# Kernel tuning notes

Hardware: AMD Instinct MI355X
Metric: run time of the kernel (lower is better)

## Reference

```python
import jax, jax.numpy as jnp
import numpy as np


def setup_inputs() -> dict:
    key = jax.random.key(0)
    k1, k2 = jax.random.split(key)
    x = jax.random.normal(k1, (16384, 1024), dtype=jnp.float32)
    # 10 butterfly stages, each with 512 independent 2x2 mixing matrices
    Ws = jax.random.normal(k2, (10, 512, 2, 2), dtype=jnp.float32)
    return {"x": x, "Ws": Ws}


def reference(x, Ws):
    """PairLinear_MixerBlock forward for input_dim == output_dim == 2^L.
    selector and reducer are Identity; only the butterfly mixing stages remain.
    """
    bs, dim = x.shape
    n_stages = Ws.shape[0]  # log2(dim)
    y = x
    for i in range(n_stages):
        stride = 2 ** i
        # y.view(-1, 2, 2**i).permute(0, 2, 1).contiguous().view(bs, -1)
        y = y.reshape(-1, 2, stride).transpose(0, 2, 1).reshape(bs, -1)
        # PairLinear: view(bs, -1, 2) then per-pair 2x2 matmul with Ws[i]
        y = jnp.einsum('bpk,pkj->bpj', y.reshape(bs, -1, 2), Ws[i]).reshape(bs, -1)
        # y.view(-1, 2**i, 2).permute(0, 2, 1).contiguous()
        y = y.reshape(-1, stride, 2).transpose(0, 2, 1).reshape(bs, dim)
    return y
```

## Files before the change

### kernel.cpp

```cpp
#include <hip/hip_runtime.h>

#define DIM 1024
#define RPW 2
#define WAVES 4
#define ROWS_PER_BLOCK (RPW * WAVES)
#define PACKED_BYTES (6 * 4 * 64 * 8 * 4)

typedef float f32x4 __attribute__((ext_vector_type(4)));


__global__ void pack_weights(const float* __restrict__ Ws, float* __restrict__ pw) {
    int t = blockIdx.x * blockDim.x + threadIdx.x;
    if (t >= 6 * 4 * 64) return;
    int lane = t & 63;
    int q = (t >> 6) & 3;
    int i = (t >> 8) + 2;
    int m = 1 << (i - 2);
    int a = (lane >> (i - 2)) & 1;
    int P0 = (((q * 64 + lane) >> (i - 1)) << i) | ((lane & (m - 1)) << 2);
    const float4* Wm = (const float4*)Ws;
    float4 wa, wb;
    float* pa = (float*)&wa;
    float* pb = (float*)&wb;
    #pragma unroll
    for (int e = 0; e < 4; ++e) {
        float4 M = Wm[i * 512 + P0 + e];
        pa[e] = a ? M.w : M.x;
        pb[e] = a ? M.y : M.z;
    }
    float4* o = (float4*)pw + (size_t)t * 2;
    o[0] = wa;
    o[1] = wb;
}

template <bool PACKED>
__global__ __launch_bounds__(256) void butterfly_kernel(
    const float* __restrict__ x,
    const float* __restrict__ Ws,
    const float* __restrict__ pw,
    float* __restrict__ out,
    int rows)
{
    const int lane = threadIdx.x & 63;
    const int wave = threadIdx.x >> 6;
    const int row0 = (blockIdx.x * WAVES + wave) * RPW;

    const float4* __restrict__ Wm = (const float4*)Ws;

    float d[RPW][16];

    #pragma unroll
    for (int r = 0; r < RPW; ++r) {
        int row = row0 + r;
        if (row < rows) {
            const f32x4* src = (const f32x4*)(x + (size_t)row * DIM);
            #pragma unroll
            for (int q = 0; q < 4; ++q) {
                f32x4 v = __builtin_nontemporal_load(&src[q * 64 + lane]);
                d[r][q*4+0] = v.x; d[r][q*4+1] = v.y;
                d[r][q*4+2] = v.z; d[r][q*4+3] = v.w;
            }
        } else {
            #pragma unroll
            for (int e = 0; e < 16; ++e) d[r][e] = 0.f;
        }
    }

    #pragma unroll
    for (int q = 0; q < 4; ++q) {
        int base = 0*512 + q*128 + lane*2;
        float4 m0 = Wm[base], m1 = Wm[base+1];
        #pragma unroll
        for (int r = 0; r < RPW; ++r) {
            int e = q*4;
            float u = d[r][e+0], v = d[r][e+1];
            d[r][e+0] = u*m0.x + v*m0.z;
            d[r][e+1] = u*m0.y + v*m0.w;
            u = d[r][e+2]; v = d[r][e+3];
            d[r][e+2] = u*m1.x + v*m1.z;
            d[r][e+3] = u*m1.y + v*m1.w;
        }
    }

    #pragma unroll
    for (int q = 0; q < 4; ++q) {
        int base = 1*512 + q*128 + lane*2;
        float4 m0 = Wm[base], m1 = Wm[base+1];
        #pragma unroll
        for (int r = 0; r < RPW; ++r) {
            int e = q*4;
            float u = d[r][e+0], v = d[r][e+2];
            d[r][e+0] = u*m0.x + v*m0.z;
            d[r][e+2] = u*m0.y + v*m0.w;
            u = d[r][e+1]; v = d[r][e+3];
            d[r][e+1] = u*m1.x + v*m1.z;
            d[r][e+3] = u*m1.y + v*m1.w;
        }
    }

    #pragma unroll
    for (int i = 2; i < 8; ++i) {
        const int m = 1 << (i - 2);
        #pragma unroll
        for (int q = 0; q < 4; ++q) {
            float wA0, wA1, wA2, wA3, wB0, wB1, wB2, wB3;
            if (PACKED) {
                const float4* wp = (const float4*)pw
                    + ((size_t)(((i - 2) * 4 + q) * 64 + lane)) * 2;
                float4 wa = wp[0], wb = wp[1];
                wA0 = wa.x; wA1 = wa.y; wA2 = wa.z; wA3 = wa.w;
                wB0 = wb.x; wB1 = wb.y; wB2 = wb.z; wB3 = wb.w;
            } else {
                const int a = (lane >> (i - 2)) & 1;
                int P0 = (((q*64 + lane) >> (i-1)) << i) | ((lane & (m-1)) << 2);
                int base = i*512 + P0;
                float4 M0 = Wm[base+0], M1 = Wm[base+1], M2 = Wm[base+2], M3 = Wm[base+3];
                wA0 = a ? M0.w : M0.x; wB0 = a ? M0.y : M0.z;
                wA1 = a ? M1.w : M1.x; wB1 = a ? M1.y : M1.z;
                wA2 = a ? M2.w : M2.x; wB2 = a ? M2.y : M2.z;
                wA3 = a ? M3.w : M3.x; wB3 = a ? M3.y : M3.z;
            }
            #pragma unroll
            for (int r = 0; r < RPW; ++r) {
                int e = q*4;
                float o0 = __shfl_xor(d[r][e+0], m);
                float o1 = __shfl_xor(d[r][e+1], m);
                float o2 = __shfl_xor(d[r][e+2], m);
                float o3 = __shfl_xor(d[r][e+3], m);
                d[r][e+0] = d[r][e+0]*wA0 + o0*wB0;
                d[r][e+1] = d[r][e+1]*wA1 + o1*wB1;
                d[r][e+2] = d[r][e+2]*wA2 + o2*wB2;
                d[r][e+3] = d[r][e+3]*wA3 + o3*wB3;
            }
        }
    }

    #pragma unroll
    for (int qp = 0; qp < 2; ++qp) {
        int base = 8*512 + qp*256 + lane*4;
        float4 M0 = Wm[base+0], M1 = Wm[base+1], M2 = Wm[base+2], M3 = Wm[base+3];
        #pragma unroll
        for (int r = 0; r < RPW; ++r) {
            int eu = (2*qp)*4, ev = (2*qp+1)*4;
            float u, v;
            u = d[r][eu+0]; v = d[r][ev+0]; d[r][eu+0] = u*M0.x + v*M0.z; d[r][ev+0] = u*M0.y + v*M0.w;
            u = d[r][eu+1]; v = d[r][ev+1]; d[r][eu+1] = u*M1.x + v*M1.z; d[r][ev+1] = u*M1.y + v*M1.w;
            u = d[r][eu+2]; v = d[r][ev+2]; d[r][eu+2] = u*M2.x + v*M2.z; d[r][ev+2] = u*M2.y + v*M2.w;
            u = d[r][eu+3]; v = d[r][ev+3]; d[r][eu+3] = u*M3.x + v*M3.z; d[r][ev+3] = u*M3.y + v*M3.w;
        }
    }

    #pragma unroll
    for (int qp = 0; qp < 2; ++qp) {
        int base = 9*512 + qp*256 + lane*4;
        float4 M0 = Wm[base+0], M1 = Wm[base+1], M2 = Wm[base+2], M3 = Wm[base+3];
        #pragma unroll
        for (int r = 0; r < RPW; ++r) {
            int eu = qp*4, ev = (qp+2)*4;
            float u, v;
            u = d[r][eu+0]; v = d[r][ev+0]; d[r][eu+0] = u*M0.x + v*M0.z; d[r][ev+0] = u*M0.y + v*M0.w;
            u = d[r][eu+1]; v = d[r][ev+1]; d[r][eu+1] = u*M1.x + v*M1.z; d[r][ev+1] = u*M1.y + v*M1.w;
            u = d[r][eu+2]; v = d[r][ev+2]; d[r][eu+2] = u*M2.x + v*M2.z; d[r][ev+2] = u*M2.y + v*M2.w;
            u = d[r][eu+3]; v = d[r][ev+3]; d[r][eu+3] = u*M3.x + v*M3.z; d[r][ev+3] = u*M3.y + v*M3.w;
        }
    }

    #pragma unroll
    for (int r = 0; r < RPW; ++r) {
        int row = row0 + r;
        if (row < rows) {
            f32x4* dst = (f32x4*)(out + (size_t)row * DIM);
            #pragma unroll
            for (int q = 0; q < 4; ++q) {
                f32x4 v;
                v.x = d[r][q*4+0]; v.y = d[r][q*4+1];
                v.z = d[r][q*4+2]; v.w = d[r][q*4+3];
                __builtin_nontemporal_store(v, &dst[q * 64 + lane]);
            }
        }
    }
}

extern "C" void kernel_launch(void* const* d_in, const int* in_sizes, int n_in,
                              void* d_out, int out_size, void* d_ws, size_t ws_size,
                              hipStream_t stream) {
    const float* x  = (const float*)d_in[0];
    const float* Ws = (const float*)d_in[1];
    float* out = (float*)d_out;

    int rows = in_sizes[0] / DIM;
    int grid = (rows + ROWS_PER_BLOCK - 1) / ROWS_PER_BLOCK;

    if (ws_size >= (size_t)PACKED_BYTES) {
        float* pw = (float*)d_ws;
        pack_weights<<<6, 256, 0, stream>>>(Ws, pw);
        butterfly_kernel<true><<<grid, 256, 0, stream>>>(x, Ws, pw, out, rows);
    } else {
        butterfly_kernel<false><<<grid, 256, 0, stream>>>(x, Ws, nullptr, out, rows);
    }
}
```

Before: 47.00 us.

## Process two 4-row tiles per wave with loads issued before compute

Restructures the kernel so each wave owns two tiles of four rows, loading both tiles up front and then computing and storing each in turn. This amortizes per-stage weight loads across more rows and puts more global loads in flight per wave. In exchange it greatly raises register use and shrinks the grid, reducing occupancy. It also drops handling for row counts not divisible by four.

New measurement: 49.95 us. +6.3%, slower.

```diff
diff --git a/kernel.cpp b/kernel.cpp
--- a/kernel.cpp
+++ b/kernel.cpp
@@ -1,9 +1,9 @@
 #include <hip/hip_runtime.h>
 
 #define DIM 1024
-#define RPW 2
+#define RPT 4
 #define WAVES 4
-#define ROWS_PER_BLOCK (RPW * WAVES)
+#define TILES_PER_WAVE 2
 #define PACKED_BYTES (6 * 4 * 64 * 8 * 4)
 
 typedef float f32x4 __attribute__((ext_vector_type(4)));
@@ -33,45 +33,46 @@
     o[1] = wb;
 }
 
+__device__ __forceinline__ void load_tile(const float* __restrict__ x, int tile,
+                                          int lane, float (&d)[RPT][16]) {
+    const f32x4* src = (const f32x4*)(x + (size_t)tile * RPT * DIM);
+    #pragma unroll
+    for (int r = 0; r < RPT; ++r) {
+        #pragma unroll
+        for (int q = 0; q < 4; ++q) {
+            f32x4 v = __builtin_nontemporal_load(&src[r * 256 + q * 64 + lane]);
+            d[r][q*4+0] = v.x; d[r][q*4+1] = v.y;
+            d[r][q*4+2] = v.z; d[r][q*4+3] = v.w;
+        }
+    }
+}
+
+__device__ __forceinline__ void store_tile(float* __restrict__ out, int tile,
+                                           int lane, float (&d)[RPT][16]) {
+    f32x4* dst = (f32x4*)(out + (size_t)tile * RPT * DIM);
+    #pragma unroll
+    for (int r = 0; r < RPT; ++r) {
+        #pragma unroll
+        for (int q = 0; q < 4; ++q) {
+            f32x4 v;
+            v.x = d[r][q*4+0]; v.y = d[r][q*4+1];
+            v.z = d[r][q*4+2]; v.w = d[r][q*4+3];
+            __builtin_nontemporal_store(v, &dst[r * 256 + q * 64 + lane]);
+        }
+    }
+}
+
 template <bool PACKED>
-__global__ __launch_bounds__(256) void butterfly_kernel(
-    const float* __restrict__ x,
-    const float* __restrict__ Ws,
-    const float* __restrict__ pw,
-    float* __restrict__ out,
-    int rows)
-{
-    const int lane = threadIdx.x & 63;
-    const int wave = threadIdx.x >> 6;
-    const int row0 = (blockIdx.x * WAVES + wave) * RPW;
-
-    const float4* __restrict__ Wm = (const float4*)Ws;
-
-    float d[RPW][16];
-
-    #pragma unroll
-    for (int r = 0; r < RPW; ++r) {
-        int row = row0 + r;
-        if (row < rows) {
-            const f32x4* src = (const f32x4*)(x + (size_t)row * DIM);
-            #pragma unroll
-            for (int q = 0; q < 4; ++q) {
-                f32x4 v = __builtin_nontemporal_load(&src[q * 64 + lane]);
-                d[r][q*4+0] = v.x; d[r][q*4+1] = v.y;
-                d[r][q*4+2] = v.z; d[r][q*4+3] = v.w;
-            }
-        } else {
-            #pragma unroll
-            for (int e = 0; e < 16; ++e) d[r][e] = 0.f;
-        }
-    }
-
+__device__ __forceinline__ void compute_tile(float (&d)[RPT][16],
+                                             const float4* __restrict__ Wm,
+                                             const float* __restrict__ pw,
+                                             int lane) {
     #pragma unroll
     for (int q = 0; q < 4; ++q) {
         int base = 0*512 + q*128 + lane*2;
         float4 m0 = Wm[base], m1 = Wm[base+1];
         #pragma unroll
-        for (int r = 0; r < RPW; ++r) {
+        for (int r = 0; r < RPT; ++r) {
             int e = q*4;
             float u = d[r][e+0], v = d[r][e+1];
             d[r][e+0] = u*m0.x + v*m0.z;
@@ -87,7 +88,7 @@
         int base = 1*512 + q*128 + lane*2;
         float4 m0 = Wm[base], m1 = Wm[base+1];
         #pragma unroll
-        for (int r = 0; r < RPW; ++r) {
+        for (int r = 0; r < RPT; ++r) {
             int e = q*4;
             float u = d[r][e+0], v = d[r][e+2];
             d[r][e+0] = u*m0.x + v*m0.z;
@@ -121,7 +122,7 @@
                 wA3 = a ? M3.w : M3.x; wB3 = a ? M3.y : M3.z;
             }
             #pragma unroll
-            for (int r = 0; r < RPW; ++r) {
+            for (int r = 0; r < RPT; ++r) {
                 int e = q*4;
                 float o0 = __shfl_xor(d[r][e+0], m);
                 float o1 = __shfl_xor(d[r][e+1], m);
@@ -140,7 +141,7 @@
         int base = 8*512 + qp*256 + lane*4;
         float4 M0 = Wm[base+0], M1 = Wm[base+1], M2 = Wm[base+2], M3 = Wm[base+3];
         #pragma unroll
-        for (int r = 0; r < RPW; ++r) {
+        for (int r = 0; r < RPT; ++r) {
             int eu = (2*qp)*4, ev = (2*qp+1)*4;
             float u, v;
             u = d[r][eu+0]; v = d[r][ev+0]; d[r][eu+0] = u*M0.x + v*M0.z; d[r][ev+0] = u*M0.y + v*M0.w;
@@ -155,7 +156,7 @@
         int base = 9*512 + qp*256 + lane*4;
         float4 M0 = Wm[base+0], M1 = Wm[base+1], M2 = Wm[base+2], M3 = Wm[base+3];
         #pragma unroll
-        for (int r = 0; r < RPW; ++r) {
+        for (int r = 0; r < RPT; ++r) {
             int eu = qp*4, ev = (qp+2)*4;
             float u, v;
             u = d[r][eu+0]; v = d[r][ev+0]; d[r][eu+0] = u*M0.x + v*M0.z; d[r][ev+0] = u*M0.y + v*M0.w;
@@ -164,20 +165,38 @@
             u = d[r][eu+3]; v = d[r][ev+3]; d[r][eu+3] = u*M3.x + v*M3.z; d[r][ev+3] = u*M3.y + v*M3.w;
         }
     }
-
-    #pragma unroll
-    for (int r = 0; r < RPW; ++r) {
-        int row = row0 + r;
-        if (row < rows) {
-            f32x4* dst = (f32x4*)(out + (size_t)row * DIM);
-            #pragma unroll
-            for (int q = 0; q < 4; ++q) {
-                f32x4 v;
-                v.x = d[r][q*4+0]; v.y = d[r][q*4+1];
-                v.z = d[r][q*4+2]; v.w = d[r][q*4+3];
-                __builtin_nontemporal_store(v, &dst[q * 64 + lane]);
-            }
-        }
+}
+
+template <bool PACKED>
+__global__ __launch_bounds__(256) void butterfly_kernel(
+    const float* __restrict__ x,
+    const float* __restrict__ Ws,
+    const float* __restrict__ pw,
+    float* __restrict__ out,
+    int ntiles)
+{
+    const int lane = threadIdx.x & 63;
+    const int wave = threadIdx.x >> 6;
+    const int g = blockIdx.x * WAVES + wave;
+    const int tA = g * TILES_PER_WAVE;
+    const int tB = tA + 1;
+
+    const float4* __restrict__ Wm = (const float4*)Ws;
+
+    float dA[RPT][16], dB[RPT][16];
+    const bool hasA = tA < ntiles;
+    const bool hasB = tB < ntiles;
+
+    if (hasA) load_tile(x, tA, lane, dA);
+    if (hasB) load_tile(x, tB, lane, dB);
+
+    if (hasA) {
+        compute_tile<PACKED>(dA, Wm, pw, lane);
+        store_tile(out, tA, lane, dA);
+    }
+    if (hasB) {
+        compute_tile<PACKED>(dB, Wm, pw, lane);
+        store_tile(out, tB, lane, dB);
     }
 }
 
@@ -189,13 +208,15 @@
     float* out = (float*)d_out;
 
     int rows = in_sizes[0] / DIM;
-    int grid = (rows + ROWS_PER_BLOCK - 1) / ROWS_PER_BLOCK;
+    int ntiles = rows / RPT;
+    int tiles_per_block = WAVES * TILES_PER_WAVE;
+    int grid = (ntiles + tiles_per_block - 1) / tiles_per_block;
 
     if (ws_size >= (size_t)PACKED_BYTES) {
         float* pw = (float*)d_ws;
         pack_weights<<<6, 256, 0, stream>>>(Ws, pw);
-        butterfly_kernel<true><<<grid, 256, 0, stream>>>(x, Ws, pw, out, rows);
+        butterfly_kernel<true><<<grid, 256, 0, stream>>>(x, Ws, pw, out, ntiles);
     } else {
-        butterfly_kernel<false><<<grid, 256, 0, stream>>>(x, Ws, nullptr, out, rows);
-    }
-}
+        butterfly_kernel<false><<<grid, 256, 0, stream>>>(x, Ws, nullptr, out, ntiles);
+    }
+}
```
